# Performance work log

Measured on AMD Instinct MI355X. Metric: run time of the kernel, lower is better.

Reference implementation:

```python
import jax, jax.numpy as jnp
import numpy as np

NEG_SLOPE = 0.2
ZTOL = 1e-9
INF = 1e12


def _gat_forward(x, a, W, S):
    # x: [B,G,N], a: [P,E,2F], W: [P,E,F,G], S: [E,N,N]
    B, G, N = x.shape
    P, E, twoF = a.shape
    F = W.shape[2]
    # self-loops added ONLY for the attention mask (faithful to source:
    # learnAttentionGSO modifies S locally; graphAttention's final matmul uses original S)
    S_I = S + jnp.eye(N, dtype=S.dtype)[None]
    Wx = jnp.einsum('pefg,bgn->bpefn', W, x)  # [B,P,E,F,N]
    a1, a2 = a[..., :F], a[..., F:]
    s1 = jnp.einsum('pef,bpefn->bpen', a1, Wx)  # varies along j (columns)
    s2 = jnp.einsum('pef,bpefn->bpen', a2, Wx)  # varies along i (rows)
    e = s1[:, :, :, None, :] + s2[:, :, :, :, None]  # [B,P,E,N,N], e[...,i,j]
    e = jnp.where(e >= 0, e, NEG_SLOPE * e)  # leaky relu
    mask = (jnp.sum(jnp.abs(S_I), axis=0) > ZTOL).astype(x.dtype)  # [N,N]
    scores = e * mask - (1.0 - mask) * INF
    aij = jax.nn.softmax(scores, axis=-1) * mask  # [B,P,E,N,N]
    # y_i = sum_e sum_j s_ij^e * alpha_ij * W x_j  (original S, no self-loop)
    y = jnp.einsum('bpefm,bpemn->bpfn', Wx, S[None, None] * aij)  # [B,P,F,N]
    y = jax.nn.relu(y)
    # concatenate heads: [B,P,F,N] -> [B, P*F, N]
    return y.transpose(0, 3, 1, 2).reshape(B, N, P * F).transpose(0, 2, 1)


def setup_inputs() -> dict:
    key = jax.random.key(0)
    k1, k2, k3, k4, k5 = jax.random.split(key, 5)
    B, G, N, P, E, F = 4, 128, 2048, 4, 1, 64
    x = jax.random.normal(k1, (B, G, N), dtype=jnp.float32)
    stdv = 1.0 / np.sqrt(G * P)  # matches reset_parameters
    a = jax.random.uniform(k2, (P, E, 2 * F), jnp.float32, -stdv, stdv)
    W = jax.random.uniform(k3, (P, E, F, G), jnp.float32, -stdv, stdv)
    density = 0.05
    Svals = jax.random.normal(k4, (E, N, N), dtype=jnp.float32)
    Smask = (jax.random.uniform(k5, (E, N, N)) < density).astype(jnp.float32)
    S = Svals * Smask
    return {"x": x, "a": a, "W": W, "S": S}


def reference(x, a, W, S):
    return _gat_forward(x, a, W, S)
```

## Files before the change

### kernel.cpp

```cpp
#include <hip/hip_runtime.h>
#include <hip/hip_bf16.h>

typedef unsigned short u16;
typedef unsigned int u32;

#define NEG_SLOPE 0.2f
#define ZTOLF 1e-9f
#define CAP 256

typedef __attribute__((ext_vector_type(4))) float f32x4;
typedef __attribute__((ext_vector_type(8))) short bf16x8;

__device__ __forceinline__ float b2f(u16 v) {
  return __uint_as_float(((u32)v) << 16);
}
__device__ __forceinline__ u16 f2b(float f) {
  u32 u = __float_as_uint(f);
  return (u16)((u + 0x7fffu + ((u >> 16) & 1u)) >> 16);
}
__device__ __forceinline__ float ldin(const void* p, size_t i, int isbf) {
  return isbf ? b2f(((const u16*)p)[i]) : ((const float*)p)[i];
}

__global__ __launch_bounds__(256) void k_detect(const u32* __restrict__ xw,
                                                u32* __restrict__ flag,
                                                uint4* __restrict__ cnt_p4) {
  __shared__ u32 cnt_s[4];
  const int tid = threadIdx.x;
  const uint4 z = make_uint4(0u, 0u, 0u, 0u);
  for (int i = tid; i < 8192; i += 256) cnt_p4[i] = z;
  const u32 w = xw[tid];
  const u32 e = (w >> 7) & 0xffu;
  const int in = (e >= 118u && e <= 131u) ? 1 : 0;
  unsigned long long bal = __ballot(in);
  const int lane = tid & 63, wid = tid >> 6;
  if (lane == 0) cnt_s[wid] = (u32)__popcll(bal);
  __syncthreads();
  if (tid == 0) {
    u32 tot = cnt_s[0] + cnt_s[1] + cnt_s[2] + cnt_s[3];
    flag[0] = (tot >= 128u) ? 1u : 0u;
  }
}

__global__ __launch_bounds__(256) void k_wx(const void* __restrict__ x,
                                            const void* __restrict__ W,
                                            const void* __restrict__ a,
                                            u16* __restrict__ Wx,
                                            float* __restrict__ s1t,
                                            float* __restrict__ s2t,
                                            const u32* __restrict__ flag) {
  __shared__ float smem_f[64 * 68 + 64 * 64];
  const int isbf = (int)flag[0];
  const int tid = threadIdx.x;
  const int n0 = blockIdx.x * 64;
  const int bp = blockIdx.y;
  const int b = bp >> 2, p = bp & 3;

  if (isbf) {
    u16* XsT = (u16*)smem_f;
    const u16* xb = (const u16*)x + (size_t)b * 128 * 2048;
    const u16* Wb = (const u16*)W + (size_t)p * 64 * 128;
#pragma unroll
    for (int j = 0; j < 4; ++j) {
      const int idx = tid + j * 256;
      const int g = idx >> 3, ng = (idx & 7) * 8;
      uint4 pk = *(const uint4*)(xb + (size_t)g * 2048 + n0 + ng);
      u16 e[8];
      e[0] = (u16)(pk.x & 0xffffu); e[1] = (u16)(pk.x >> 16);
      e[2] = (u16)(pk.y & 0xffffu); e[3] = (u16)(pk.y >> 16);
      e[4] = (u16)(pk.z & 0xffffu); e[5] = (u16)(pk.z >> 16);
      e[6] = (u16)(pk.w & 0xffffu); e[7] = (u16)(pk.w >> 16);
#pragma unroll
      for (int i = 0; i < 8; ++i) XsT[(ng + i) * 136 + g] = e[i];
    }
    __syncthreads();
    const int lane = tid & 63, wv = tid >> 6;
    const int f0 = wv * 16;
    const int arow = lane & 15, kgrp = lane >> 4;
    f32x4 zero = {0.f, 0.f, 0.f, 0.f};
    f32x4 acc[4] = {zero, zero, zero, zero};
#pragma unroll
    for (int kb = 0; kb < 4; ++kb) {
      bf16x8 afrag = *(const bf16x8*)(Wb + (size_t)(f0 + arow) * 128 + kb * 32 + kgrp * 8);
#pragma unroll
      for (int t = 0; t < 4; ++t) {
        bf16x8 bfrag = *(const bf16x8*)&XsT[(t * 16 + arow) * 136 + kb * 32 + kgrp * 8];
        acc[t] = __builtin_amdgcn_mfma_f32_16x16x32_bf16(afrag, bfrag, acc[t], 0, 0, 0);
      }
    }
    float a1v[4], a2v[4];
#pragma unroll
    for (int v = 0; v < 4; ++v) {
      a1v[v] = b2f(((const u16*)a)[p * 128 + f0 + kgrp * 4 + v]);
      a2v[v] = b2f(((const u16*)a)[p * 128 + 64 + f0 + kgrp * 4 + v]);
    }
    __syncthreads();
    float* red1 = smem_f;
    float* red2 = smem_f + 64 * 17;
#pragma unroll
    for (int t = 0; t < 4; ++t) {
      const int n_l = t * 16 + arow;
      u32 lo = (u32)f2b(acc[t][0]) | ((u32)f2b(acc[t][1]) << 16);
      u32 hi = (u32)f2b(acc[t][2]) | ((u32)f2b(acc[t][3]) << 16);
      *(uint2*)(Wx + ((size_t)(bp * 2048 + n0 + n_l) * 64 + f0 + kgrp * 4)) = make_uint2(lo, hi);
      float p1 = a1v[0] * acc[t][0] + a1v[1] * acc[t][1] + a1v[2] * acc[t][2] + a1v[3] * acc[t][3];
      float p2 = a2v[0] * acc[t][0] + a2v[1] * acc[t][1] + a2v[2] * acc[t][2] + a2v[3] * acc[t][3];
      red1[n_l * 17 + wv * 4 + kgrp] = p1;
      red2[n_l * 17 + wv * 4 + kgrp] = p2;
    }
    __syncthreads();
    if (tid < 64) {
      float v1 = 0.f, v2 = 0.f;
#pragma unroll
      for (int k = 0; k < 16; ++k) {
        v1 += red1[tid * 17 + k];
        v2 += red2[tid * 17 + k];
      }
      s1t[(size_t)(n0 + tid) * 16 + bp] = v1;
      s2t[(size_t)(n0 + tid) * 16 + bp] = v2;
    }
    return;
  }

  float* Wt = smem_f;
  float* Xs = smem_f + 64 * 68;
  const int tn = tid & 15, tf = tid >> 4;
  float acc[4][4] = {{0.f}};
  const size_t Wbase = (size_t)p * 64 * 128;
  const size_t xbase = (size_t)b * 128 * 2048;
  for (int kt = 0; kt < 2; ++kt) {
    const int g0 = kt * 64;
#pragma unroll
    for (int j = 0; j < 16; ++j) {
      int idx = tid + j * 256;
      int f = idx >> 6, g = idx & 63;
      Wt[g * 68 + f] = ((const float*)W)[Wbase + (size_t)f * 128 + g0 + g];
    }
#pragma unroll
    for (int j = 0; j < 16; ++j) {
      int idx = tid + j * 256;
      int g = idx >> 6, nn = idx & 63;
      Xs[g * 64 + nn] = ((const float*)x)[xbase + (size_t)(g0 + g) * 2048 + n0 + nn];
    }
    __syncthreads();
#pragma unroll 4
    for (int g = 0; g < 64; ++g) {
      float4 wv = *(const float4*)&Wt[g * 68 + tf * 4];
      float4 xv = *(const float4*)&Xs[g * 64 + tn * 4];
      acc[0][0] += wv.x * xv.x; acc[0][1] += wv.x * xv.y; acc[0][2] += wv.x * xv.z; acc[0][3] += wv.x * xv.w;
      acc[1][0] += wv.y * xv.x; acc[1][1] += wv.y * xv.y; acc[1][2] += wv.y * xv.z; acc[1][3] += wv.y * xv.w;
      acc[2][0] += wv.z * xv.x; acc[2][1] += wv.z * xv.y; acc[2][2] += wv.z * xv.z; acc[2][3] += wv.z * xv.w;
      acc[3][0] += wv.w * xv.x; acc[3][1] += wv.w * xv.y; acc[3][2] += wv.w * xv.z; acc[3][3] += wv.w * xv.w;
    }
    __syncthreads();
  }
#pragma unroll
  for (int j = 0; j < 4; ++j) {
    int n = n0 + tn * 4 + j;
    u32 lo = (u32)f2b(acc[0][j]) | ((u32)f2b(acc[1][j]) << 16);
    u32 hi = (u32)f2b(acc[2][j]) | ((u32)f2b(acc[3][j]) << 16);
    *(uint2*)(Wx + ((size_t)(bp * 2048 + n) * 64 + tf * 4)) = make_uint2(lo, hi);
  }
  float a1v[4], a2v[4];
#pragma unroll
  for (int fi = 0; fi < 4; ++fi) {
    a1v[fi] = ((const float*)a)[(size_t)p * 128 + tf * 4 + fi];
    a2v[fi] = ((const float*)a)[(size_t)p * 128 + 64 + tf * 4 + fi];
  }
  float* red1 = Wt;
  float* red2 = Wt + 64 * 17;
#pragma unroll
  for (int j = 0; j < 4; ++j) {
    float p1 = a1v[0] * acc[0][j] + a1v[1] * acc[1][j] + a1v[2] * acc[2][j] + a1v[3] * acc[3][j];
    float p2 = a2v[0] * acc[0][j] + a2v[1] * acc[1][j] + a2v[2] * acc[2][j] + a2v[3] * acc[3][j];
    red1[(tn * 4 + j) * 17 + tf] = p1;
    red2[(tn * 4 + j) * 17 + tf] = p2;
  }
  __syncthreads();
  if (tid < 64) {
    float v1 = 0.f, v2 = 0.f;
#pragma unroll
    for (int k = 0; k < 16; ++k) {
      v1 += red1[tid * 17 + k];
      v2 += red2[tid * 17 + k];
    }
    s1t[(size_t)(n0 + tid) * 16 + bp] = v1;
    s2t[(size_t)(n0 + tid) * 16 + bp] = v2;
  }
}

__global__ __launch_bounds__(256) void k_csc(const void* __restrict__ S,
                                             u32* __restrict__ cnt_p,
                                             u32* __restrict__ col_m,
                                             float* __restrict__ col_v,
                                             const float* __restrict__ s1t,
                                             const float* __restrict__ s2t,
                                             float4* __restrict__ stat3,
                                             const u32* __restrict__ flag) {
  __shared__ u32 wsum[4];
  __shared__ u32 ls_n[CAP];
  __shared__ u32 c2s;
  __shared__ float red[256];
  __shared__ float Mred[16];
  const int isbf = (int)flag[0];
  const int m = blockIdx.x;
  const int tid = threadIdx.x;
  const int lane = tid & 63, wid = tid >> 6;
  const int n0 = tid * 8;
  float v[8];
  if (isbf) {
    uint4 pk = ((const uint4*)S)[(size_t)m * 256 + tid];
    u32 wv[4] = {pk.x, pk.y, pk.z, pk.w};
#pragma unroll
    for (int j = 0; j < 4; ++j) {
      v[2 * j]     = b2f((u16)(wv[j] & 0xffffu));
      v[2 * j + 1] = b2f((u16)(wv[j] >> 16));
    }
  } else {
    float4 f0 = ((const float4*)S)[(size_t)m * 512 + 2 * tid];
    float4 f1 = ((const float4*)S)[(size_t)m * 512 + 2 * tid + 1];
    v[0] = f0.x; v[1] = f0.y; v[2] = f0.z; v[3] = f0.w;
    v[4] = f1.x; v[5] = f1.y; v[6] = f1.z; v[7] = f1.w;
  }
  u32 rflags = 0, rc = 0;
#pragma unroll
  for (int j = 0; j < 8; ++j) {
    const int n = n0 + j;
    const float svd = (n == m) ? v[j] + 1.f : v[j];
    if (fabsf(svd) > ZTOLF) { rflags |= 1u << j; rc++; }
  }
  u32 inc = rc;
#pragma unroll
  for (int off = 1; off < 64; off <<= 1) {
    u32 y = __shfl_up(inc, off);
    if (lane >= off) inc += y;
  }
  if (lane == 63) wsum[wid] = inc;
  __syncthreads();
  u32 wbase = 0;
#pragma unroll
  for (int k = 0; k < 4; ++k) wbase += (k < wid) ? wsum[k] : 0u;
  u32 pos = wbase + inc - rc;
#pragma unroll
  for (int j = 0; j < 8; ++j) {
    if ((rflags >> j) & 1u) {
      if (pos < CAP) ls_n[pos] = (u32)(n0 + j);
      pos++;
    }
  }
  if (tid == 255) c2s = min(wbase + inc, (u32)CAP);
#pragma unroll
  for (int j = 0; j < 8; ++j) {
    const float sv = v[j];
    if (sv != 0.f) {
      const int n = n0 + j;
      u32 slot = atomicAdd(&cnt_p[(size_t)n * 16], 1u);
      if (slot < CAP) {
        col_m[(size_t)n * CAP + slot] = (u32)m;
        col_v[(size_t)n * CAP + slot] = sv;
      }
    }
  }
  __syncthreads();
  const int c2 = (int)c2s;
  const int bp = tid & 15, sub = tid >> 4;
  const float s2v = s2t[(size_t)m * 16 + bp];
  float ev[16];
  float mymax = -3e38f;
#pragma unroll
  for (int k = 0; k < 16; ++k) {
    const int i = sub + k * 16;
    float e = -3e38f;
    if (i < c2) {
      const int nn = (int)ls_n[i];
      float s1 = s1t[(size_t)nn * 16 + bp];
      e = s1 + s2v;
      e = e >= 0.f ? e : NEG_SLOPE * e;
    }
    ev[k] = e;
    mymax = fmaxf(mymax, e);
  }
  red[tid] = mymax;
  __syncthreads();
  if (tid < 16) {
    float M = -3e38f;
#pragma unroll
    for (int s = 0; s < 16; ++s) M = fmaxf(M, red[s * 16 + tid]);
    Mred[tid] = M;
  }
  __syncthreads();
  const float M = Mred[bp];
  float ssum = 0.f;
#pragma unroll
  for (int k = 0; k < 16; ++k) ssum += __expf(ev[k] - M);
  __syncthreads();
  red[tid] = ssum;
  __syncthreads();
  if (tid < 16) {
    float Sm = 0.f;
#pragma unroll
    for (int s = 0; s < 16; ++s) Sm += red[s * 16 + tid];
    const float Mv = Mred[tid];
    const bool any = (Mv > -1e38f);
    const float rmx = any ? Mv : 0.f;
    const float inv = any ? 1.f / Sm : 0.f;
    const float s2o = s2t[(size_t)m * 16 + tid];
    stat3[(size_t)m * 16 + tid] = make_float4(s2o, rmx, inv, 0.f);
  }
}

__global__ __launch_bounds__(256, 8) void k_out(const u16* __restrict__ Wx,
                                                const u32* __restrict__ cnt_p,
                                                const u32* __restrict__ col_m,
                                                const float* __restrict__ col_v,
                                                const float* __restrict__ s1t,
                                                const float4* __restrict__ stat3,
                                                void* __restrict__ out,
                                                const u32* __restrict__ flag) {
  __shared__ u32 lds_m[CAP + 8];
  __shared__ float lds_v[CAP + 8];
  __shared__ float lds_w[(CAP + 8) * 4];
  __shared__ float lds_r[3 * 256];
  __shared__ float s1s4[4];
  const int isbf = (int)flag[0];
  const int tid = threadIdx.x;
  const int bid = blockIdx.x;
  const int xcd = bid & 7, lin = bid >> 3;
  const int bpg = xcd >> 1;
  const int n = ((xcd & 1) << 10) | lin;
  const int c = min((int)cnt_p[(size_t)n * 16], CAP);
  const int cpad = (c + 15) & ~15;
  if (tid < 4) s1s4[tid] = s1t[(size_t)n * 16 + bpg * 4 + tid];
  for (int t2 = tid; t2 < cpad + 8; t2 += 256) {
    lds_m[t2] = (t2 < c) ? col_m[(size_t)n * CAP + t2] : 0u;
    lds_v[t2] = (t2 < c) ? col_v[(size_t)n * CAP + t2] : 0.f;
  }
  __syncthreads();
  const int totk = (cpad + 8) * 4;
  for (int k = tid; k < totk; k += 256) {
    const int i = k >> 2, bp4 = k & 3;
    const int bp = bpg * 4 + bp4;
    float w = 0.f;
    if (i < c) {
      const int mm = (int)lds_m[i];
      const float sv = lds_v[i];
      const float svd = (mm == n) ? sv + 1.f : sv;
      if (fabsf(svd) > ZTOLF) {
        float4 s = stat3[(size_t)mm * 16 + bp];
        float e = s1s4[bp4] + s.x;
        e = e >= 0.f ? e : NEG_SLOPE * e;
        w = sv * __expf(e - s.y) * s.z;
      }
    }
    lds_w[k] = w;
  }
  __syncthreads();
  const int lane = tid & 63, h = tid >> 6;
  const int e2 = lane >> 5;
  const int bp4 = (lane >> 3) & 3;
  const int bp = bpg * 4 + bp4;
  const int f8 = lane & 7;
  const u16* wxp = Wx + (size_t)bp * (2048 * 64) + f8 * 8;
  float acc[8] = {0.f, 0.f, 0.f, 0.f, 0.f, 0.f, 0.f, 0.f};
  int i = h * 2 + e2;
  u32 mmA = lds_m[i];
  float wA = lds_w[i * 4 + bp4];
  uint4 dA = *(const uint4*)(wxp + (size_t)mmA * 64);
  for (int base = 0; base < cpad; base += 16) {
    const int iB = i + 8;
    const u32 mmB = lds_m[iB];
    const float wB = lds_w[iB * 4 + bp4];
    const uint4 dB = *(const uint4*)(wxp + (size_t)mmB * 64);
    acc[0] += wA * b2f((u16)(dA.x & 0xffffu)); acc[1] += wA * b2f((u16)(dA.x >> 16));
    acc[2] += wA * b2f((u16)(dA.y & 0xffffu)); acc[3] += wA * b2f((u16)(dA.y >> 16));
    acc[4] += wA * b2f((u16)(dA.z & 0xffffu)); acc[5] += wA * b2f((u16)(dA.z >> 16));
    acc[6] += wA * b2f((u16)(dA.w & 0xffffu)); acc[7] += wA * b2f((u16)(dA.w >> 16));
    i = iB + 8;
    mmA = lds_m[i];
    wA = lds_w[i * 4 + bp4];
    dA = *(const uint4*)(wxp + (size_t)mmA * 64);
    acc[0] += wB * b2f((u16)(dB.x & 0xffffu)); acc[1] += wB * b2f((u16)(dB.x >> 16));
    acc[2] += wB * b2f((u16)(dB.y & 0xffffu)); acc[3] += wB * b2f((u16)(dB.y >> 16));
    acc[4] += wB * b2f((u16)(dB.z & 0xffffu)); acc[5] += wB * b2f((u16)(dB.z >> 16));
    acc[6] += wB * b2f((u16)(dB.w & 0xffffu)); acc[7] += wB * b2f((u16)(dB.w >> 16));
  }
#pragma unroll
  for (int k = 0; k < 8; ++k) acc[k] += __shfl_xor(acc[k], 32);
  if (h > 0 && e2 == 0) {
    float* dst = &lds_r[(h - 1) * 256 + bp4 * 64 + f8 * 8];
    *(float4*)dst = make_float4(acc[0], acc[1], acc[2], acc[3]);
    *(float4*)(dst + 4) = make_float4(acc[4], acc[5], acc[6], acc[7]);
  }
  __syncthreads();
  if (h == 0 && e2 == 0) {
#pragma unroll
    for (int q = 0; q < 3; ++q) {
      const float* src = &lds_r[q * 256 + bp4 * 64 + f8 * 8];
#pragma unroll
      for (int k = 0; k < 8; ++k) acc[k] += src[k];
    }
    const size_t r0 = (size_t)(bp * 64 + f8 * 8);
    if (isbf) {
      u16* ob = (u16*)out;
#pragma unroll
      for (int k = 0; k < 8; ++k) ob[(r0 + k) * 2048 + n] = f2b(fmaxf(acc[k], 0.f));
    } else {
      float* of = (float*)out;
#pragma unroll
      for (int k = 0; k < 8; ++k) of[(r0 + k) * 2048 + n] = fmaxf(acc[k], 0.f);
    }
  }
}

extern "C" void kernel_launch(void* const* d_in, const int* in_sizes, int n_in,
                              void* d_out, int out_size, void* d_ws, size_t ws_size,
                              hipStream_t stream) {
  const void* x = d_in[0];
  const void* a = d_in[1];
  const void* W = d_in[2];
  const void* S = d_in[3];

  char* ws = (char*)d_ws;
  u16* Wx      = (u16*)ws;
  float* s1t   = (float*)(ws + 4u * 1024 * 1024);
  float* s2t   = s1t + 2048 * 16;
  float4* stat3= (float4*)(s2t + 2048 * 16);
  u32* cnt_p   = (u32*)((char*)stat3 + 512u * 1024);
  u32* col_m   = cnt_p + 2048 * 16;
  float* col_v = (float*)(col_m + 2048 * CAP);
  u32* flag    = (u32*)(col_v + 2048 * CAP);

  k_detect<<<1, 256, 0, stream>>>((const u32*)x, flag, (uint4*)cnt_p);
  k_wx<<<dim3(32, 16), 256, 0, stream>>>(x, W, a, Wx, s1t, s2t, flag);
  k_csc<<<2048, 256, 0, stream>>>(S, cnt_p, col_m, col_v, s1t, s2t, stat3, flag);
  k_out<<<8192, 256, 0, stream>>>(Wx, cnt_p, col_m, col_v, s1t, stat3, d_out, flag);
}
```

Baseline: 129.6 us.

## Build column CSC lists in a dedicated tiled kernel instead of per-element atomics

Moves construction of the per-column nonzero lists out of k_csc into a new k_colbuild kernel. It stages 512x32 tiles of S in LDS, counts nonzeros per column, and reserves slots with one atomic per column per tile instead of one global atomic per nonzero. The aim is to cut global atomic contention and make the output ordering deterministic within a tile. The cost is a second full read of S and an extra kernel launch, and the large LDS footprint limits occupancy.

New measurement: 136.4 us. 1.05x slower.

```diff
diff --git a/kernel.cpp b/kernel.cpp
--- a/kernel.cpp
+++ b/kernel.cpp
@@ -189,10 +189,91 @@
   }
 }
 
+__global__ __launch_bounds__(256) void k_colbuild(const void* __restrict__ S,
+                                                  u32* __restrict__ cnt_p,
+                                                  u32* __restrict__ col_m,
+                                                  float* __restrict__ col_v,
+                                                  const u32* __restrict__ flag) {
+  __shared__ u32 tbuf[16896];
+  __shared__ u32 scnt[32 * 9];
+  __shared__ u32 gbase[32];
+  const int isbf = (int)flag[0];
+  const int tid = threadIdx.x;
+  const int n0 = blockIdx.x * 32;
+  const int m0 = blockIdx.y * 512;
+  if (isbf) {
+    u16* t16 = (u16*)tbuf;
+    const u16* Sb = (const u16*)S;
+#pragma unroll
+    for (int rr = 0; rr < 2; ++rr) {
+      const int r = tid * 2 + rr;
+      const u16* src = Sb + (size_t)(m0 + r) * 2048 + n0;
+      uint4 A = *(const uint4*)(src);
+      uint4 B = *(const uint4*)(src + 8);
+      uint4 C = *(const uint4*)(src + 16);
+      uint4 D = *(const uint4*)(src + 24);
+      u32* dst = (u32*)(t16 + r * 34);
+      dst[0] = A.x; dst[1] = A.y; dst[2] = A.z; dst[3] = A.w;
+      dst[4] = B.x; dst[5] = B.y; dst[6] = B.z; dst[7] = B.w;
+      dst[8] = C.x; dst[9] = C.y; dst[10] = C.z; dst[11] = C.w;
+      dst[12] = D.x; dst[13] = D.y; dst[14] = D.z; dst[15] = D.w;
+    }
+  } else {
+    float* t32 = (float*)tbuf;
+    const float* Sf = (const float*)S;
+#pragma unroll
+    for (int rr = 0; rr < 2; ++rr) {
+      const int r = tid * 2 + rr;
+      const float* src = Sf + (size_t)(m0 + r) * 2048 + n0;
+      float* dst = t32 + r * 33;
+#pragma unroll
+      for (int q = 0; q < 8; ++q) {
+        float4 v4 = *(const float4*)(src + q * 4);
+        dst[q * 4 + 0] = v4.x; dst[q * 4 + 1] = v4.y;
+        dst[q * 4 + 2] = v4.z; dst[q * 4 + 3] = v4.w;
+      }
+    }
+  }
+  __syncthreads();
+  const int j = tid & 31, s = tid >> 5;
+  const u16* t16 = (const u16*)tbuf;
+  const float* t32 = (const float*)tbuf;
+  u32 cnt = 0;
+#pragma unroll 8
+  for (int k = 0; k < 64; ++k) {
+    const int r = s + k * 8;
+    const float v = isbf ? b2f(t16[r * 34 + j]) : t32[r * 33 + j];
+    if (v != 0.f) cnt++;
+  }
+  scnt[j * 9 + s] = cnt;
+  __syncthreads();
+  if (tid < 32) {
+    u32 tot = 0;
+#pragma unroll
+    for (int ss = 0; ss < 8; ++ss) {
+      u32 c = scnt[tid * 9 + ss];
+      scnt[tid * 9 + ss] = tot;
+      tot += c;
+    }
+    gbase[tid] = atomicAdd(&cnt_p[(size_t)(n0 + tid) * 16], tot);
+  }
+  __syncthreads();
+  u32 off = gbase[j] + scnt[j * 9 + s];
+#pragma unroll 8
+  for (int k = 0; k < 64; ++k) {
+    const int r = s + k * 8;
+    const float v = isbf ? b2f(t16[r * 34 + j]) : t32[r * 33 + j];
+    if (v != 0.f) {
+      if (off < CAP) {
+        col_m[(size_t)(n0 + j) * CAP + off] = (u32)(m0 + r);
+        col_v[(size_t)(n0 + j) * CAP + off] = v;
+      }
+      off++;
+    }
+  }
+}
+
 __global__ __launch_bounds__(256) void k_csc(const void* __restrict__ S,
-                                             u32* __restrict__ cnt_p,
-                                             u32* __restrict__ col_m,
-                                             float* __restrict__ col_v,
                                              const float* __restrict__ s1t,
                                              const float* __restrict__ s2t,
                                              float4* __restrict__ stat3,
@@ -249,18 +330,6 @@
     }
   }
   if (tid == 255) c2s = min(wbase + inc, (u32)CAP);
-#pragma unroll
-  for (int j = 0; j < 8; ++j) {
-    const float sv = v[j];
-    if (sv != 0.f) {
-      const int n = n0 + j;
-      u32 slot = atomicAdd(&cnt_p[(size_t)n * 16], 1u);
-      if (slot < CAP) {
-        col_m[(size_t)n * CAP + slot] = (u32)m;
-        col_v[(size_t)n * CAP + slot] = sv;
-      }
-    }
-  }
   __syncthreads();
   const int c2 = (int)c2s;
   const int bp = tid & 15, sub = tid >> 4;
@@ -285,7 +354,7 @@
   if (tid < 16) {
     float M = -3e38f;
 #pragma unroll
-    for (int s = 0; s < 16; ++s) M = fmaxf(M, red[s * 16 + tid]);
+    for (int ss = 0; ss < 16; ++ss) M = fmaxf(M, red[ss * 16 + tid]);
     Mred[tid] = M;
   }
   __syncthreads();
@@ -299,7 +368,7 @@
   if (tid < 16) {
     float Sm = 0.f;
 #pragma unroll
-    for (int s = 0; s < 16; ++s) Sm += red[s * 16 + tid];
+    for (int ss = 0; ss < 16; ++ss) Sm += red[ss * 16 + tid];
     const float Mv = Mred[tid];
     const bool any = (Mv > -1e38f);
     const float rmx = any ? Mv : 0.f;
@@ -431,7 +500,8 @@
   u32* flag    = (u32*)(col_v + 2048 * CAP);
 
   k_detect<<<1, 256, 0, stream>>>((const u32*)x, flag, (uint4*)cnt_p);
+  k_colbuild<<<dim3(64, 4), 256, 0, stream>>>(S, cnt_p, col_m, col_v, flag);
   k_wx<<<dim3(32, 16), 256, 0, stream>>>(x, W, a, Wx, s1t, s2t, flag);
-  k_csc<<<2048, 256, 0, stream>>>(S, cnt_p, col_m, col_v, s1t, s2t, stat3, flag);
+  k_csc<<<2048, 256, 0, stream>>>(S, s1t, s2t, stat3, flag);
   k_out<<<8192, 256, 0, stream>>>(Wx, cnt_p, col_m, col_v, s1t, stat3, d_out, flag);
 }
```

## Split row softmax stats into separate wave-per-row kernel using monotone max

Applied to the files above, without the earlier changes.

The per-row softmax statistics (max and sum of exp) move out of the CSC-building kernel into a new k_rows kernel, with one wavefront per row. Row neighbor lists and counts now go to global memory instead of LDS. The new kernel gets the max as leaky(s2 + max s1), which is valid because leaky ReLU is monotone. It also reads s1 as float4 and reduces across the wave with shuffles, so several block barriers go away. The cost is an extra kernel launch plus global writes and reads of the row lists.

After: 137.9 us. 1.06x slower.

```diff
diff --git a/kernel.cpp b/kernel.cpp
--- a/kernel.cpp
+++ b/kernel.cpp
@@ -24,11 +24,13 @@
 
 __global__ __launch_bounds__(256) void k_detect(const u32* __restrict__ xw,
                                                 u32* __restrict__ flag,
-                                                uint4* __restrict__ cnt_p4) {
+                                                uint4* __restrict__ cnt_p4,
+                                                uint4* __restrict__ rcnt4) {
   __shared__ u32 cnt_s[4];
   const int tid = threadIdx.x;
   const uint4 z = make_uint4(0u, 0u, 0u, 0u);
   for (int i = tid; i < 8192; i += 256) cnt_p4[i] = z;
+  for (int i = tid; i < 512; i += 256) rcnt4[i] = z;
   const u32 w = xw[tid];
   const u32 e = (w >> 7) & 0xffu;
   const int in = (e >= 118u && e <= 131u) ? 1 : 0;
@@ -193,15 +195,10 @@
                                              u32* __restrict__ cnt_p,
                                              u32* __restrict__ col_m,
                                              float* __restrict__ col_v,
-                                             const float* __restrict__ s1t,
-                                             const float* __restrict__ s2t,
-                                             float4* __restrict__ stat3,
+                                             u32* __restrict__ rcnt,
+                                             u32* __restrict__ row_n,
                                              const u32* __restrict__ flag) {
   __shared__ u32 wsum[4];
-  __shared__ u32 ls_n[CAP];
-  __shared__ u32 c2s;
-  __shared__ float red[256];
-  __shared__ float Mred[16];
   const int isbf = (int)flag[0];
   const int m = blockIdx.x;
   const int tid = threadIdx.x;
@@ -244,11 +241,11 @@
 #pragma unroll
   for (int j = 0; j < 8; ++j) {
     if ((rflags >> j) & 1u) {
-      if (pos < CAP) ls_n[pos] = (u32)(n0 + j);
+      if (pos < CAP) row_n[(size_t)m * CAP + pos] = (u32)(n0 + j);
       pos++;
     }
   }
-  if (tid == 255) c2s = min(wbase + inc, (u32)CAP);
+  if (tid == 255) rcnt[m] = min(wbase + inc, (u32)CAP);
 #pragma unroll
   for (int j = 0; j < 8; ++j) {
     const float sv = v[j];
@@ -261,52 +258,64 @@
       }
     }
   }
-  __syncthreads();
-  const int c2 = (int)c2s;
-  const int bp = tid & 15, sub = tid >> 4;
-  const float s2v = s2t[(size_t)m * 16 + bp];
-  float ev[16];
-  float mymax = -3e38f;
-#pragma unroll
-  for (int k = 0; k < 16; ++k) {
-    const int i = sub + k * 16;
-    float e = -3e38f;
-    if (i < c2) {
-      const int nn = (int)ls_n[i];
-      float s1 = s1t[(size_t)nn * 16 + bp];
-      e = s1 + s2v;
-      e = e >= 0.f ? e : NEG_SLOPE * e;
-    }
-    ev[k] = e;
-    mymax = fmaxf(mymax, e);
-  }
-  red[tid] = mymax;
-  __syncthreads();
-  if (tid < 16) {
-    float M = -3e38f;
-#pragma unroll
-    for (int s = 0; s < 16; ++s) M = fmaxf(M, red[s * 16 + tid]);
-    Mred[tid] = M;
-  }
-  __syncthreads();
-  const float M = Mred[bp];
-  float ssum = 0.f;
-#pragma unroll
-  for (int k = 0; k < 16; ++k) ssum += __expf(ev[k] - M);
-  __syncthreads();
-  red[tid] = ssum;
-  __syncthreads();
-  if (tid < 16) {
-    float Sm = 0.f;
-#pragma unroll
-    for (int s = 0; s < 16; ++s) Sm += red[s * 16 + tid];
-    const float Mv = Mred[tid];
-    const bool any = (Mv > -1e38f);
-    const float rmx = any ? Mv : 0.f;
-    const float inv = any ? 1.f / Sm : 0.f;
-    const float s2o = s2t[(size_t)m * 16 + tid];
-    stat3[(size_t)m * 16 + tid] = make_float4(s2o, rmx, inv, 0.f);
-  }
+}
+
+__global__ __launch_bounds__(256) void k_rows(const u32* __restrict__ rcnt,
+                                              const u32* __restrict__ row_n,
+                                              const float* __restrict__ s1t,
+                                              const float* __restrict__ s2t,
+                                              float4* __restrict__ stat3) {
+  const int tid = threadIdx.x;
+  const int lane = tid & 63, wv = tid >> 6;
+  const int m = blockIdx.x * 4 + wv;
+  const int c2 = min((int)rcnt[m], CAP);
+  int ne[4];
+#pragma unroll
+  for (int I = 0; I < 4; ++I) {
+    int i = lane + I * 64;
+    ne[I] = (i < c2) ? (int)row_n[(size_t)m * CAP + i] : -1;
+  }
+  const float s2v = (lane < 16) ? s2t[(size_t)m * 16 + lane] : 0.f;
+  float my_rmx = 0.f, my_inv = 0.f;
+#pragma unroll
+  for (int g = 0; g < 4; ++g) {
+    float4 sg[4];
+#pragma unroll
+    for (int I = 0; I < 4; ++I)
+      sg[I] = (ne[I] >= 0) ? *(const float4*)&s1t[(size_t)ne[I] * 16 + g * 4]
+                           : make_float4(-3e38f, -3e38f, -3e38f, -3e38f);
+#pragma unroll
+    for (int q = 0; q < 4; ++q) {
+      const int bp = g * 4 + q;
+      const float s2m = __shfl(s2v, bp);
+      float s1max = -3e38f;
+#pragma unroll
+      for (int I = 0; I < 4; ++I) {
+        float xv = (q == 0) ? sg[I].x : (q == 1) ? sg[I].y : (q == 2) ? sg[I].z : sg[I].w;
+        s1max = fmaxf(s1max, xv);
+      }
+#pragma unroll
+      for (int off = 32; off; off >>= 1) s1max = fmaxf(s1max, __shfl_xor(s1max, off));
+      float rmx = s2m + s1max;
+      rmx = rmx >= 0.f ? rmx : NEG_SLOPE * rmx;
+      float sm = 0.f;
+#pragma unroll
+      for (int I = 0; I < 4; ++I) {
+        float xv = (q == 0) ? sg[I].x : (q == 1) ? sg[I].y : (q == 2) ? sg[I].z : sg[I].w;
+        float e = xv + s2m;
+        e = e >= 0.f ? e : NEG_SLOPE * e;
+        sm += __expf(e - rmx);
+      }
+#pragma unroll
+      for (int off = 32; off; off >>= 1) sm += __shfl_xor(sm, off);
+      const bool any = (s1max > -1e38f);
+      const float rmxo = any ? rmx : 0.f;
+      const float inv = any ? 1.f / sm : 0.f;
+      if (lane == bp) { my_rmx = rmxo; my_inv = inv; }
+    }
+  }
+  if (lane < 16)
+    stat3[(size_t)m * 16 + lane] = make_float4(s2v, my_rmx, my_inv, 0.f);
 }
 
 __global__ __launch_bounds__(256, 8) void k_out(const u16* __restrict__ Wx,
@@ -426,12 +435,15 @@
   float* s2t   = s1t + 2048 * 16;
   float4* stat3= (float4*)(s2t + 2048 * 16);
   u32* cnt_p   = (u32*)((char*)stat3 + 512u * 1024);
-  u32* col_m   = cnt_p + 2048 * 16;
+  u32* rcnt    = cnt_p + 2048 * 16;
+  u32* col_m   = rcnt + 2048;
   float* col_v = (float*)(col_m + 2048 * CAP);
-  u32* flag    = (u32*)(col_v + 2048 * CAP);
-
-  k_detect<<<1, 256, 0, stream>>>((const u32*)x, flag, (uint4*)cnt_p);
+  u32* row_n   = (u32*)(col_v + 2048 * CAP);
+  u32* flag    = row_n + 2048 * CAP;
+
+  k_detect<<<1, 256, 0, stream>>>((const u32*)x, flag, (uint4*)cnt_p, (uint4*)rcnt);
   k_wx<<<dim3(32, 16), 256, 0, stream>>>(x, W, a, Wx, s1t, s2t, flag);
-  k_csc<<<2048, 256, 0, stream>>>(S, cnt_p, col_m, col_v, s1t, s2t, stat3, flag);
+  k_csc<<<2048, 256, 0, stream>>>(S, cnt_p, col_m, col_v, rcnt, row_n, flag);
+  k_rows<<<512, 256, 0, stream>>>(rcnt, row_n, s1t, s2t, stat3);
   k_out<<<8192, 256, 0, stream>>>(Wx, cnt_p, col_m, col_v, s1t, stat3, d_out, flag);
 }
```
